# Performance work log

Hardware: AMD Instinct MI355X
Metric: run time of the kernel (lower is better)

The kernel has to match this reference:

```python
import jax, jax.numpy as jnp
import numpy as np

N_USERS = 100000
N_ITEMS = 50000
N_NODES = N_USERS + N_ITEMS
EMB_DIM = 64
N_EDGES = 4000000
N_LAYERS = 3
BATCH = 4096


def setup_inputs() -> dict:
    key = jax.random.key(0)
    k = jax.random.split(key, 7)
    return {
        "user_emb": jax.random.normal(k[0], (N_USERS, EMB_DIM), dtype=jnp.float32) * 0.1,
        "item_emb": jax.random.normal(k[1], (N_ITEMS, EMB_DIM), dtype=jnp.float32) * 0.1,
        "vals": jax.random.uniform(k[2], (N_EDGES,), dtype=jnp.float32),
        "src": jax.random.randint(k[3], (N_EDGES,), 0, N_NODES, dtype=jnp.int32),
        "dst": jax.random.randint(k[4], (N_EDGES,), 0, N_NODES, dtype=jnp.int32),
        "users": jax.random.randint(k[5], (BATCH,), 0, N_USERS, dtype=jnp.int32),
        "items": jax.random.randint(k[6], (BATCH,), 0, N_ITEMS, dtype=jnp.int32),
    }


def _propagate(user_emb, item_emb, vals, src, dst):
    # all_emb: [N, D]; sparse adjacency A given as COO (src -> dst, weight vals)
    all_emb = jnp.concatenate([user_emb, item_emb], axis=0)
    acc = all_emb  # running sum over layers (layer 0 included)
    emb = all_emb
    for _ in range(N_LAYERS):
        # SpMM: out[d] = sum_{e: dst[e]==d} vals[e] * emb[src[e]]
        msgs = vals[:, None] * emb[src]               # [E, D]
        emb = jax.ops.segment_sum(msgs, dst, num_segments=N_NODES)
        acc = acc + emb
    light_out = acc / jnp.float32(N_LAYERS + 1)       # mean over stacked layers
    return light_out[:N_USERS], light_out[N_USERS:]


def reference(user_emb, item_emb, vals, src, dst, users, items):
    all_users, all_items = _propagate(user_emb, item_emb, vals, src, dst)
    u = all_users[users]                              # [B, D]
    i = all_items[items]                              # [B, D]
    gamma = jnp.sum(u * i, axis=1)                    # [B]
    return gamma
```

## Files before the change

### kernel.cpp

```cpp
#include <hip/hip_runtime.h>
#include <hip/hip_bf16.h>

#define N_USERS 100000
#define N_ITEMS 50000
#define N_NODES 150000
#define DIM 64
#define N_EDGES 4000000
#define BATCH 4096

#define NBKT 512
#define BW 294
#define STRIDE 9216
#define PA_EDGES 4096
#define PA_ITER 16

__device__ __forceinline__ float blo(unsigned int u) { return __uint_as_float(u << 16); }
__device__ __forceinline__ float bhi(unsigned int u) { return __uint_as_float(u & 0xffff0000u); }
__device__ __forceinline__ unsigned int f2b(float f) {
    unsigned int x = __float_as_uint(f);
    return (x + 0x7fffu + ((x >> 16) & 1u)) >> 16;
}
__device__ __forceinline__ unsigned int pack2(float a, float b) {
    return f2b(a) | (f2b(b) << 16);
}

typedef float v2f __attribute__((ext_vector_type(2)));

__global__ void k_markcvt(const float* __restrict__ uemb, const float* __restrict__ iemb,
                          ushort* __restrict__ out, int* __restrict__ gcur) {
    int tid = blockIdx.x * blockDim.x + threadIdx.x;
    if (tid < NBKT) gcur[tid] = 0;
    int i = tid * 4;
    if (i >= N_NODES * DIM) return;
    const float* srcp = (i < N_USERS * DIM) ? (uemb + i) : (iemb + (i - N_USERS * DIM));
    float4 v;
    v.x = __builtin_nontemporal_load(srcp + 0);
    v.y = __builtin_nontemporal_load(srcp + 1);
    v.z = __builtin_nontemporal_load(srcp + 2);
    v.w = __builtin_nontemporal_load(srcp + 3);
    *(uint2*)(out + i) = make_uint2(pack2(v.x, v.y), pack2(v.z, v.w));
}

__global__ void __launch_bounds__(256, 4) k_partition(
        const int* __restrict__ src, const int* __restrict__ dst,
        const float* __restrict__ vals,
        int* __restrict__ gcur, int2* __restrict__ tmp) {
    __shared__ int cnt[NBKT];
    __shared__ int base_s[NBKT];
    __shared__ int off_s[NBKT];
    __shared__ int2 rec_s[PA_EDGES];
    __shared__ ushort bin_s[PA_EDGES];
    int t = threadIdx.x;
    for (int i = t; i < NBKT; i += 256) cnt[i] = 0;
    __syncthreads();
    size_t base = (size_t)blockIdx.x * PA_EDGES;
    int myb[PA_ITER];
    int mykey[PA_ITER];
    int myval[PA_ITER];
#pragma unroll
    for (int it = 0; it < PA_ITER; it++) {
        size_t i = base + (size_t)it * 256 + t;
        myb[it] = -1;
        if (i < N_EDGES) {
            int d = __builtin_nontemporal_load(dst + i);
            int s = __builtin_nontemporal_load(src + i);
            float v = __builtin_nontemporal_load(vals + i);
            int b = d / BW;
            int local = d - b * BW;
            myb[it] = b;
            mykey[it] = (s << 9) | local;
            myval[it] = __float_as_int(v);
            atomicAdd(&cnt[b], 1);
        }
    }
    __syncthreads();
    for (int i = t; i < NBKT; i += 256) {
        int c = cnt[i];
        base_s[i] = (c > 0) ? atomicAdd(&gcur[i], c) : 0;
    }
    if (t < 64) {
        int lane = t;
        int carry = 0;
        for (int c = 0; c < NBKT / 64; c++) {
            int i = c * 64 + lane;
            int x = cnt[i];
            int incl = x;
            for (int o = 1; o < 64; o <<= 1) {
                int y = __shfl_up(incl, o);
                if (lane >= o) incl += y;
            }
            off_s[i] = carry + incl - x;
            carry += __shfl(incl, 63);
        }
    }
    __syncthreads();
    for (int i = t; i < NBKT; i += 256) cnt[i] = 0;
    __syncthreads();
#pragma unroll
    for (int it = 0; it < PA_ITER; it++) {
        int b = myb[it];
        if (b >= 0) {
            int pos = off_s[b] + atomicAdd(&cnt[b], 1);
            rec_s[pos] = make_int2(mykey[it], myval[it]);
            bin_s[pos] = (ushort)b;
        }
    }
    __syncthreads();
    int nrec = off_s[NBKT - 1] + cnt[NBKT - 1];
    for (int i = t; i < nrec; i += 256) {
        int2 r = rec_s[i];
        int b = bin_s[i];
        tmp[(size_t)b * STRIDE + base_s[b] + (i - off_s[b])] = r;
    }
}

__global__ void k_scan(const int* __restrict__ gcur, int* __restrict__ bucket_ptr) {
    int lane = threadIdx.x;
    int carry = 0;
    for (int c = 0; c < NBKT / 64; c++) {
        int i = c * 64 + lane;
        int x = gcur[i];
        int incl = x;
        for (int off = 1; off < 64; off <<= 1) {
            int y = __shfl_up(incl, off);
            if (lane >= off) incl += y;
        }
        bucket_ptr[i] = carry + incl - x;
        carry += __shfl(incl, 63);
    }
    if (lane == 0) bucket_ptr[NBKT] = N_EDGES;
}

__global__ void k_bsort(const int2* __restrict__ tmp, const int* __restrict__ gcur,
                        const int* __restrict__ bucket_ptr, int* __restrict__ row_ptr,
                        int2* __restrict__ fin) {
    __shared__ int cnt[BW + 64];
    __shared__ int off[BW + 64];
    int b = blockIdx.x, t = threadIdx.x;
    int node0 = b * BW;
    int nodes = min(BW, N_NODES - node0);
    int gbase = bucket_ptr[b];
    int count = gcur[b];
    const int2* tb = tmp + (size_t)b * STRIDE;
    for (int i = t; i < BW + 64; i += 512) cnt[i] = 0;
    __syncthreads();
    for (int e = t; e < count; e += 512) atomicAdd(&cnt[tb[e].x & 511], 1);
    __syncthreads();
    if (t < 64) {
        int lane = t;
        int carry = 0;
        for (int c = 0; c < 5; c++) {
            int i = c * 64 + lane;
            int x = (i < nodes) ? cnt[i] : 0;
            int incl = x;
            for (int o = 1; o < 64; o <<= 1) {
                int y = __shfl_up(incl, o);
                if (lane >= o) incl += y;
            }
            if (i <= nodes) off[i] = carry + incl - x;
            carry += __shfl(incl, 63);
        }
    }
    __syncthreads();
    for (int i = t; i <= nodes; i += 512)
        if (node0 + i <= N_NODES) row_ptr[node0 + i] = gbase + off[i];
    __syncthreads();
    for (int e = t; e < count; e += 512) {
        int2 r = tb[e];
        int local = r.x & 511;
        int pos = gbase + atomicAdd(&off[local], 1);
        fin[pos] = make_int2(r.x >> 9, r.y);
    }
}


#define EDGE_FMA(r, u)                                                        \
    {                                                                         \
        float vf = __int_as_float((r).y);                                     \
        v2f vv = {vf, vf};                                                    \
        v2f f0 = {blo((u).x), bhi((u).x)};                                    \
        v2f f1 = {blo((u).y), bhi((u).y)};                                    \
        v2f f2 = {blo((u).z), bhi((u).z)};                                    \
        v2f f3 = {blo((u).w), bhi((u).w)};                                    \
        acc0 = __builtin_elementwise_fma(vv, f0, acc0);                       \
        acc1 = __builtin_elementwise_fma(vv, f1, acc1);                       \
        acc2 = __builtin_elementwise_fma(vv, f2, acc2);                       \
        acc3 = __builtin_elementwise_fma(vv, f3, acc3);                       \
    }

#define GATHER16(basec, r) (*(const uint4*)((basec) + ((((unsigned int)(r).x) << 7) | qoff)))
#define REC8(basec, i) (*(const int2*)((basec) + (((unsigned int)(i)) << 3)))

#define BURST32(basec)                                                        \
    {                                                                         \
        int e1 = e + 8, e2 = e + 16, e3 = e + 24;                             \
        int2 ra = REC8(basec, e);                                             \
        int2 rb = REC8(basec, min(e1, last));                                 \
        int2 rc = REC8(basec, min(e2, last));                                 \
        int2 rd = REC8(basec, min(e3, last));                                 \
        rb.y = (e1 < end) ? rb.y : 0;                                         \
        rc.y = (e2 < end) ? rc.y : 0;                                         \
        rd.y = (e3 < end) ? rd.y : 0;                                         \
        uint4 ua = GATHER16(einc, ra);                                        \
        uint4 ub = GATHER16(einc, rb);                                        \
        uint4 uc = GATHER16(einc, rc);                                        \
        uint4 ud = GATHER16(einc, rd);                                        \
        EDGE_FMA(ra, ua);                                                     \
        EDGE_FMA(rb, ub);                                                     \
        EDGE_FMA(rc, uc);                                                     \
        EDGE_FMA(rd, ud);                                                     \
        e += 32;                                                              \
    }

__global__ void k_spmm16(const ushort* __restrict__ ein, ushort* __restrict__ eout,
                         const int* __restrict__ row_ptr, const int2* __restrict__ fin) {
    int wave = (blockIdx.x * blockDim.x + threadIdx.x) >> 6;
    if (wave >= N_NODES) return;
    int lane = threadIdx.x & 63;
    int g = lane >> 3;
    int q = lane & 7;
    unsigned int qoff = (unsigned int)q << 4;
    const char* einc = (const char*)ein;
    const char* finc = (const char*)fin;
    int start = row_ptr[wave], end = row_ptr[wave + 1];
    int last = max(start, end - 1);
    v2f acc0 = {0.f, 0.f}, acc1 = {0.f, 0.f}, acc2 = {0.f, 0.f}, acc3 = {0.f, 0.f};
    int e = start + g;
    while (e < end) BURST32(finc);
#pragma unroll
    for (int off = 8; off < 64; off <<= 1) {
        acc0.x += __shfl_xor(acc0.x, off);
        acc0.y += __shfl_xor(acc0.y, off);
        acc1.x += __shfl_xor(acc1.x, off);
        acc1.y += __shfl_xor(acc1.y, off);
        acc2.x += __shfl_xor(acc2.x, off);
        acc2.y += __shfl_xor(acc2.y, off);
        acc3.x += __shfl_xor(acc3.x, off);
        acc3.y += __shfl_xor(acc3.y, off);
    }
    if (lane < 8) {
        uint4 p;
        p.x = pack2(acc0.x, acc0.y);
        p.y = pack2(acc1.x, acc1.y);
        p.z = pack2(acc2.x, acc2.y);
        p.w = pack2(acc3.x, acc3.y);
        *(uint4*)(eout + (size_t)wave * DIM + q * 8) = p;
    }
}

__global__ void k_samp(const ushort* __restrict__ ein, const int* __restrict__ row_ptr,
                       const int2* __restrict__ fin, const int* __restrict__ users,
                       const int* __restrict__ items, float* __restrict__ l3) {
    int slot = (blockIdx.x * blockDim.x + threadIdx.x) >> 6;
    if (slot >= 2 * BATCH) return;
    int lane = threadIdx.x & 63;
    int g = lane >> 3;
    int q = lane & 7;
    unsigned int qoff = (unsigned int)q << 4;
    const char* einc = (const char*)ein;
    const char* finc = (const char*)fin;
    int node = (slot < BATCH) ? users[slot] : (items[slot - BATCH] + N_USERS);
    int start = row_ptr[node], end = row_ptr[node + 1];
    int last = max(start, end - 1);
    v2f acc0 = {0.f, 0.f}, acc1 = {0.f, 0.f}, acc2 = {0.f, 0.f}, acc3 = {0.f, 0.f};
    int e = start + g;
    while (e < end) BURST32(finc);
#pragma unroll
    for (int off = 8; off < 64; off <<= 1) {
        acc0.x += __shfl_xor(acc0.x, off);
        acc0.y += __shfl_xor(acc0.y, off);
        acc1.x += __shfl_xor(acc1.x, off);
        acc1.y += __shfl_xor(acc1.y, off);
        acc2.x += __shfl_xor(acc2.x, off);
        acc2.y += __shfl_xor(acc2.y, off);
        acc3.x += __shfl_xor(acc3.x, off);
        acc3.y += __shfl_xor(acc3.y, off);
    }
    if (lane < 8) {
        float* row = l3 + (size_t)slot * DIM + q * 8;
        *(float4*)row = make_float4(acc0.x, acc0.y, acc1.x, acc1.y);
        *(float4*)(row + 4) = make_float4(acc2.x, acc2.y, acc3.x, acc3.y);
    }
}

__global__ void k_gacc0(const float* __restrict__ uemb, const float* __restrict__ iemb,
                        const ushort* __restrict__ emb, const int* __restrict__ users,
                        const int* __restrict__ items, float* __restrict__ accU,
                        float* __restrict__ accI) {
    int i = blockIdx.x * blockDim.x + threadIdx.x;
    if (i >= 2 * BATCH * DIM) return;
    int j = (i < BATCH * DIM) ? i : i - BATCH * DIM;
    int b = j >> 6, l = j & 63;
    if (i < BATCH * DIM) {
        int n = users[b];
        unsigned int u = emb[(size_t)n * DIM + l];
        accU[j] = uemb[(size_t)n * DIM + l] + __uint_as_float(u << 16);
    } else {
        int n = items[b];
        unsigned int u = emb[(size_t)(n + N_USERS) * DIM + l];
        accI[j] = iemb[(size_t)n * DIM + l] + __uint_as_float(u << 16);
    }
}

__global__ void k_gacc(const ushort* __restrict__ emb, const int* __restrict__ users,
                       const int* __restrict__ items, float* __restrict__ accU,
                       float* __restrict__ accI) {
    int i = blockIdx.x * blockDim.x + threadIdx.x;
    if (i >= 2 * BATCH * DIM) return;
    int j = (i < BATCH * DIM) ? i : i - BATCH * DIM;
    int b = j >> 6, l = j & 63;
    if (i < BATCH * DIM) {
        unsigned int u = emb[(size_t)users[b] * DIM + l];
        accU[j] += __uint_as_float(u << 16);
    } else {
        unsigned int u = emb[(size_t)(items[b] + N_USERS) * DIM + l];
        accI[j] += __uint_as_float(u << 16);
    }
}

__global__ void k_dot(const float* __restrict__ accU, const float* __restrict__ accI,
                      const float* __restrict__ l3, float* __restrict__ out) {
    int b = (blockIdx.x * blockDim.x + threadIdx.x) >> 6;
    if (b >= BATCH) return;
    int lane = threadIdx.x & 63;
    float aU = accU[b * 64 + lane] + l3[(size_t)b * 64 + lane];
    float aI = accI[b * 64 + lane] + l3[(size_t)(BATCH + b) * 64 + lane];
    float p = aU * aI;
    for (int off = 32; off; off >>= 1) p += __shfl_xor(p, off);
    if (lane == 0) out[b] = p * (1.0f / 16.0f);
}


extern "C" void kernel_launch(void* const* d_in, const int* in_sizes, int n_in,
                              void* d_out, int out_size, void* d_ws, size_t ws_size,
                              hipStream_t stream) {
    const float* user_emb = (const float*)d_in[0];
    const float* item_emb = (const float*)d_in[1];
    const float* vals = (const float*)d_in[2];
    const int* src = (const int*)d_in[3];
    const int* dst = (const int*)d_in[4];
    const int* users = (const int*)d_in[5];
    const int* items = (const int*)d_in[6];
    float* out = (float*)d_out;

    char* ws = (char*)d_ws;
    size_t off = 0;
    auto alloc = [&](size_t bytes) {
        char* p = ws + off;
        off += (bytes + 255) & ~(size_t)255;
        return p;
    };
    ushort* ebf0 = (ushort*)alloc((size_t)N_NODES * DIM * 2);
    ushort* ebf1 = (ushort*)alloc((size_t)N_NODES * DIM * 2);
    ushort* ebf2 = (ushort*)alloc((size_t)N_NODES * DIM * 2);
    int2* fin = (int2*)alloc((size_t)N_EDGES * 8);
    int* row_ptr = (int*)alloc((size_t)(N_NODES + 1) * 4);
    int* bucket_ptr = (int*)alloc((size_t)(NBKT + 1) * 4);
    int* gcur = (int*)alloc((size_t)NBKT * 4);
    float* l3 = (float*)alloc((size_t)2 * BATCH * DIM * 4);
    float* accU = (float*)alloc((size_t)BATCH * DIM * 4);
    float* accI = (float*)alloc((size_t)BATCH * DIM * 4);
    int2* tmp = (int2*)ebf1;

    k_markcvt<<<(N_NODES * DIM / 4 + 255) / 256, 256, 0, stream>>>(
        user_emb, item_emb, ebf0, gcur);

    int pa_blocks = (N_EDGES + PA_EDGES - 1) / PA_EDGES;
    k_partition<<<pa_blocks, 256, 0, stream>>>(src, dst, vals, gcur, tmp);
    k_scan<<<1, 64, 0, stream>>>(gcur, bucket_ptr);
    k_bsort<<<NBKT, 512, 0, stream>>>(tmp, gcur, bucket_ptr, row_ptr, fin);

    int gb = (2 * BATCH * DIM + 255) / 256;
    int spmm_blocks = (N_NODES * 64 + 255) / 256;
    k_spmm16<<<spmm_blocks, 256, 0, stream>>>(ebf0, ebf1, row_ptr, fin);
    k_gacc0<<<gb, 256, 0, stream>>>(user_emb, item_emb, ebf1, users, items, accU, accI);
    k_spmm16<<<spmm_blocks, 256, 0, stream>>>(ebf1, ebf2, row_ptr, fin);
    k_gacc<<<gb, 256, 0, stream>>>(ebf2, users, items, accU, accI);
    k_samp<<<(2 * BATCH * 64 + 255) / 256, 256, 0, stream>>>(ebf2, row_ptr, fin, users, items, l3);

    k_dot<<<(BATCH * 64 + 255) / 256, 256, 0, stream>>>(accU, accI, l3, out);
}
```

Before: 342.5 us.

## Fuse convert into partition, inline bucket scan, two rows per wave in SpMM

Merges the fp32-to-bf16 conversion into the partition kernel as extra blocks and replaces the counter-zeroing with a memset. Each bsort block now computes its own bucket base by summing the preceding counts, which removes the scan kernel. The SpMM now processes two destination rows per wave with interleaved gathers, exposing more memory-level parallelism. The cost is more registers per thread and wasted lanes when the two rows differ in length.

```diff
diff --git a/kernel.cpp b/kernel.cpp
--- a/kernel.cpp
+++ b/kernel.cpp
@@ -13,6 +13,8 @@
 #define STRIDE 9216
 #define PA_EDGES 4096
 #define PA_ITER 16
+#define PA_BLOCKS ((N_EDGES + PA_EDGES - 1) / PA_EDGES)
+#define CVT_BLOCKS (N_NODES * DIM / 4 / 256)
 
 __device__ __forceinline__ float blo(unsigned int u) { return __uint_as_float(u << 16); }
 __device__ __forceinline__ float bhi(unsigned int u) { return __uint_as_float(u & 0xffff0000u); }
@@ -26,22 +28,9 @@
 
 typedef float v2f __attribute__((ext_vector_type(2)));
 
-__global__ void k_markcvt(const float* __restrict__ uemb, const float* __restrict__ iemb,
-                          ushort* __restrict__ out, int* __restrict__ gcur) {
-    int tid = blockIdx.x * blockDim.x + threadIdx.x;
-    if (tid < NBKT) gcur[tid] = 0;
-    int i = tid * 4;
-    if (i >= N_NODES * DIM) return;
-    const float* srcp = (i < N_USERS * DIM) ? (uemb + i) : (iemb + (i - N_USERS * DIM));
-    float4 v;
-    v.x = __builtin_nontemporal_load(srcp + 0);
-    v.y = __builtin_nontemporal_load(srcp + 1);
-    v.z = __builtin_nontemporal_load(srcp + 2);
-    v.w = __builtin_nontemporal_load(srcp + 3);
-    *(uint2*)(out + i) = make_uint2(pack2(v.x, v.y), pack2(v.z, v.w));
-}
-
-__global__ void __launch_bounds__(256, 4) k_partition(
+__global__ void __launch_bounds__(256, 4) k_cvtpart(
+        const float* __restrict__ uemb, const float* __restrict__ iemb,
+        ushort* __restrict__ ebf0,
         const int* __restrict__ src, const int* __restrict__ dst,
         const float* __restrict__ vals,
         int* __restrict__ gcur, int2* __restrict__ tmp) {
@@ -51,6 +40,19 @@
     __shared__ int2 rec_s[PA_EDGES];
     __shared__ ushort bin_s[PA_EDGES];
     int t = threadIdx.x;
+    if (blockIdx.x >= PA_BLOCKS) {
+        int tid = (blockIdx.x - PA_BLOCKS) * 256 + t;
+        int i = tid * 4;
+        if (i >= N_NODES * DIM) return;
+        const float* srcp = (i < N_USERS * DIM) ? (uemb + i) : (iemb + (i - N_USERS * DIM));
+        float4 v;
+        v.x = __builtin_nontemporal_load(srcp + 0);
+        v.y = __builtin_nontemporal_load(srcp + 1);
+        v.z = __builtin_nontemporal_load(srcp + 2);
+        v.w = __builtin_nontemporal_load(srcp + 3);
+        *(uint2*)(ebf0 + i) = make_uint2(pack2(v.x, v.y), pack2(v.z, v.w));
+        return;
+    }
     for (int i = t; i < NBKT; i += 256) cnt[i] = 0;
     __syncthreads();
     size_t base = (size_t)blockIdx.x * PA_EDGES;
@@ -114,36 +116,29 @@
     }
 }
 
-__global__ void k_scan(const int* __restrict__ gcur, int* __restrict__ bucket_ptr) {
-    int lane = threadIdx.x;
-    int carry = 0;
-    for (int c = 0; c < NBKT / 64; c++) {
-        int i = c * 64 + lane;
-        int x = gcur[i];
-        int incl = x;
-        for (int off = 1; off < 64; off <<= 1) {
-            int y = __shfl_up(incl, off);
-            if (lane >= off) incl += y;
-        }
-        bucket_ptr[i] = carry + incl - x;
-        carry += __shfl(incl, 63);
-    }
-    if (lane == 0) bucket_ptr[NBKT] = N_EDGES;
-}
-
 __global__ void k_bsort(const int2* __restrict__ tmp, const int* __restrict__ gcur,
-                        const int* __restrict__ bucket_ptr, int* __restrict__ row_ptr,
-                        int2* __restrict__ fin) {
+                        int* __restrict__ row_ptr, int2* __restrict__ fin) {
     __shared__ int cnt[BW + 64];
     __shared__ int off[BW + 64];
+    __shared__ int gbase_s;
     int b = blockIdx.x, t = threadIdx.x;
     int node0 = b * BW;
     int nodes = min(BW, N_NODES - node0);
-    int gbase = bucket_ptr[b];
     int count = gcur[b];
     const int2* tb = tmp + (size_t)b * STRIDE;
+    if (t < 64) {
+        int ssum = 0;
+#pragma unroll
+        for (int j = 0; j < 8; j++) {
+            int idx = t * 8 + j;
+            if (idx < b) ssum += gcur[idx];
+        }
+        for (int o = 32; o; o >>= 1) ssum += __shfl_xor(ssum, o);
+        if (t == 0) gbase_s = ssum;
+    }
     for (int i = t; i < BW + 64; i += 512) cnt[i] = 0;
     __syncthreads();
+    int gbase = gbase_s;
     for (int e = t; e < count; e += 512) atomicAdd(&cnt[tb[e].x & 511], 1);
     __syncthreads();
     if (t < 64) {
@@ -174,7 +169,7 @@
 }
 
 
-#define EDGE_FMA(r, u)                                                        \
+#define EDGE_FMA(r, u, A0, A1, A2, A3)                                        \
     {                                                                         \
         float vf = __int_as_float((r).y);                                     \
         v2f vv = {vf, vf};                                                    \
@@ -182,69 +177,98 @@
         v2f f1 = {blo((u).y), bhi((u).y)};                                    \
         v2f f2 = {blo((u).z), bhi((u).z)};                                    \
         v2f f3 = {blo((u).w), bhi((u).w)};                                    \
-        acc0 = __builtin_elementwise_fma(vv, f0, acc0);                       \
-        acc1 = __builtin_elementwise_fma(vv, f1, acc1);                       \
-        acc2 = __builtin_elementwise_fma(vv, f2, acc2);                       \
-        acc3 = __builtin_elementwise_fma(vv, f3, acc3);                       \
+        A0 = __builtin_elementwise_fma(vv, f0, A0);                           \
+        A1 = __builtin_elementwise_fma(vv, f1, A1);                           \
+        A2 = __builtin_elementwise_fma(vv, f2, A2);                           \
+        A3 = __builtin_elementwise_fma(vv, f3, A3);                           \
     }
 
 #define GATHER16(basec, r) (*(const uint4*)((basec) + ((((unsigned int)(r).x) << 7) | qoff)))
 #define REC8(basec, i) (*(const int2*)((basec) + (((unsigned int)(i)) << 3)))
 
-#define BURST32(basec)                                                        \
-    {                                                                         \
-        int e1 = e + 8, e2 = e + 16, e3 = e + 24;                             \
-        int2 ra = REC8(basec, e);                                             \
-        int2 rb = REC8(basec, min(e1, last));                                 \
-        int2 rc = REC8(basec, min(e2, last));                                 \
-        int2 rd = REC8(basec, min(e3, last));                                 \
-        rb.y = (e1 < end) ? rb.y : 0;                                         \
-        rc.y = (e2 < end) ? rc.y : 0;                                         \
-        rd.y = (e3 < end) ? rd.y : 0;                                         \
-        uint4 ua = GATHER16(einc, ra);                                        \
-        uint4 ub = GATHER16(einc, rb);                                        \
-        uint4 uc = GATHER16(einc, rc);                                        \
-        uint4 ud = GATHER16(einc, rd);                                        \
-        EDGE_FMA(ra, ua);                                                     \
-        EDGE_FMA(rb, ub);                                                     \
-        EDGE_FMA(rc, uc);                                                     \
-        EDGE_FMA(rd, ud);                                                     \
-        e += 32;                                                              \
-    }
-
-__global__ void k_spmm16(const ushort* __restrict__ ein, ushort* __restrict__ eout,
-                         const int* __restrict__ row_ptr, const int2* __restrict__ fin) {
+__global__ void __launch_bounds__(256) k_spmm16(
+        const ushort* __restrict__ ein, ushort* __restrict__ eout,
+        const int* __restrict__ row_ptr, const int2* __restrict__ fin) {
     int wave = (blockIdx.x * blockDim.x + threadIdx.x) >> 6;
-    if (wave >= N_NODES) return;
+    if (wave >= N_NODES / 2) return;
     int lane = threadIdx.x & 63;
     int g = lane >> 3;
     int q = lane & 7;
     unsigned int qoff = (unsigned int)q << 4;
     const char* einc = (const char*)ein;
     const char* finc = (const char*)fin;
-    int start = row_ptr[wave], end = row_ptr[wave + 1];
-    int last = max(start, end - 1);
-    v2f acc0 = {0.f, 0.f}, acc1 = {0.f, 0.f}, acc2 = {0.f, 0.f}, acc3 = {0.f, 0.f};
-    int e = start + g;
-    while (e < end) BURST32(finc);
+    int n0 = wave * 2;
+    int s0 = row_ptr[n0];
+    int m0 = row_ptr[n0 + 1];
+    int m1 = row_ptr[n0 + 2];
+    int last0 = max(s0, m0 - 1);
+    int last1 = max(m0, m1 - 1);
+    v2f A0 = {0.f, 0.f}, A1 = {0.f, 0.f}, A2 = {0.f, 0.f}, A3 = {0.f, 0.f};
+    v2f B0 = {0.f, 0.f}, B1 = {0.f, 0.f}, B2 = {0.f, 0.f}, B3 = {0.f, 0.f};
+    int ea = s0 + g, eb = m0 + g;
+    while (ea < m0 || eb < m1) {
+        int2 ra0 = REC8(finc, min(ea, last0));
+        int2 ra1 = REC8(finc, min(ea + 8, last0));
+        int2 ra2 = REC8(finc, min(ea + 16, last0));
+        int2 ra3 = REC8(finc, min(ea + 24, last0));
+        int2 rb0 = REC8(finc, min(eb, last1));
+        int2 rb1 = REC8(finc, min(eb + 8, last1));
+        int2 rb2 = REC8(finc, min(eb + 16, last1));
+        int2 rb3 = REC8(finc, min(eb + 24, last1));
+        ra0.y = (ea < m0) ? ra0.y : 0;
+        ra1.y = (ea + 8 < m0) ? ra1.y : 0;
+        ra2.y = (ea + 16 < m0) ? ra2.y : 0;
+        ra3.y = (ea + 24 < m0) ? ra3.y : 0;
+        rb0.y = (eb < m1) ? rb0.y : 0;
+        rb1.y = (eb + 8 < m1) ? rb1.y : 0;
+        rb2.y = (eb + 16 < m1) ? rb2.y : 0;
+        rb3.y = (eb + 24 < m1) ? rb3.y : 0;
+        uint4 ua0 = GATHER16(einc, ra0);
+        uint4 ua1 = GATHER16(einc, ra1);
+        uint4 ua2 = GATHER16(einc, ra2);
+        uint4 ua3 = GATHER16(einc, ra3);
+        uint4 ub0 = GATHER16(einc, rb0);
+        uint4 ub1 = GATHER16(einc, rb1);
+        uint4 ub2 = GATHER16(einc, rb2);
+        uint4 ub3 = GATHER16(einc, rb3);
+        EDGE_FMA(ra0, ua0, A0, A1, A2, A3);
+        EDGE_FMA(ra1, ua1, A0, A1, A2, A3);
+        EDGE_FMA(ra2, ua2, A0, A1, A2, A3);
+        EDGE_FMA(ra3, ua3, A0, A1, A2, A3);
+        EDGE_FMA(rb0, ub0, B0, B1, B2, B3);
+        EDGE_FMA(rb1, ub1, B0, B1, B2, B3);
+        EDGE_FMA(rb2, ub2, B0, B1, B2, B3);
+        EDGE_FMA(rb3, ub3, B0, B1, B2, B3);
+        ea += 32;
+        eb += 32;
+    }
 #pragma unroll
     for (int off = 8; off < 64; off <<= 1) {
-        acc0.x += __shfl_xor(acc0.x, off);
-        acc0.y += __shfl_xor(acc0.y, off);
-        acc1.x += __shfl_xor(acc1.x, off);
-        acc1.y += __shfl_xor(acc1.y, off);
-        acc2.x += __shfl_xor(acc2.x, off);
-        acc2.y += __shfl_xor(acc2.y, off);
-        acc3.x += __shfl_xor(acc3.x, off);
-        acc3.y += __shfl_xor(acc3.y, off);
-    }
-    if (lane < 8) {
+        A0.x += __shfl_xor(A0.x, off);
+        A0.y += __shfl_xor(A0.y, off);
+        A1.x += __shfl_xor(A1.x, off);
+        A1.y += __shfl_xor(A1.y, off);
+        A2.x += __shfl_xor(A2.x, off);
+        A2.y += __shfl_xor(A2.y, off);
+        A3.x += __shfl_xor(A3.x, off);
+        A3.y += __shfl_xor(A3.y, off);
+        B0.x += __shfl_xor(B0.x, off);
+        B0.y += __shfl_xor(B0.y, off);
+        B1.x += __shfl_xor(B1.x, off);
+        B1.y += __shfl_xor(B1.y, off);
+        B2.x += __shfl_xor(B2.x, off);
+        B2.y += __shfl_xor(B2.y, off);
+        B3.x += __shfl_xor(B3.x, off);
+        B3.y += __shfl_xor(B3.y, off);
+    }
+    if (lane < 16) {
+        bool r0 = lane < 8;
         uint4 p;
-        p.x = pack2(acc0.x, acc0.y);
-        p.y = pack2(acc1.x, acc1.y);
-        p.z = pack2(acc2.x, acc2.y);
-        p.w = pack2(acc3.x, acc3.y);
-        *(uint4*)(eout + (size_t)wave * DIM + q * 8) = p;
+        p.x = r0 ? pack2(A0.x, A0.y) : pack2(B0.x, B0.y);
+        p.y = r0 ? pack2(A1.x, A1.y) : pack2(B1.x, B1.y);
+        p.z = r0 ? pack2(A2.x, A2.y) : pack2(B2.x, B2.y);
+        p.w = r0 ? pack2(A3.x, A3.y) : pack2(B3.x, B3.y);
+        *(uint4*)(eout + (size_t)n0 * DIM + (size_t)(lane & 15) * 8) = p;
     }
 }
 
@@ -262,24 +286,42 @@
     int node = (slot < BATCH) ? users[slot] : (items[slot - BATCH] + N_USERS);
     int start = row_ptr[node], end = row_ptr[node + 1];
     int last = max(start, end - 1);
-    v2f acc0 = {0.f, 0.f}, acc1 = {0.f, 0.f}, acc2 = {0.f, 0.f}, acc3 = {0.f, 0.f};
+    v2f A0 = {0.f, 0.f}, A1 = {0.f, 0.f}, A2 = {0.f, 0.f}, A3 = {0.f, 0.f};
     int e = start + g;
-    while (e < end) BURST32(finc);
+    while (e < end) {
+        int e1 = e + 8, e2 = e + 16, e3 = e + 24;
+        int2 ra = REC8(finc, e);
+        int2 rb = REC8(finc, min(e1, last));
+        int2 rc = REC8(finc, min(e2, last));
+        int2 rd = REC8(finc, min(e3, last));
+        rb.y = (e1 < end) ? rb.y : 0;
+        rc.y = (e2 < end) ? rc.y : 0;
+        rd.y = (e3 < end) ? rd.y : 0;
+        uint4 ua = GATHER16(einc, ra);
+        uint4 ub = GATHER16(einc, rb);
+        uint4 uc = GATHER16(einc, rc);
+        uint4 ud = GATHER16(einc, rd);
+        EDGE_FMA(ra, ua, A0, A1, A2, A3);
+        EDGE_FMA(rb, ub, A0, A1, A2, A3);
+        EDGE_FMA(rc, uc, A0, A1, A2, A3);
+        EDGE_FMA(rd, ud, A0, A1, A2, A3);
+        e += 32;
+    }
 #pragma unroll
     for (int off = 8; off < 64; off <<= 1) {
-        acc0.x += __shfl_xor(acc0.x, off);
-        acc0.y += __shfl_xor(acc0.y, off);
-        acc1.x += __shfl_xor(acc1.x, off);
-        acc1.y += __shfl_xor(acc1.y, off);
-        acc2.x += __shfl_xor(acc2.x, off);
-        acc2.y += __shfl_xor(acc2.y, off);
-        acc3.x += __shfl_xor(acc3.x, off);
-        acc3.y += __shfl_xor(acc3.y, off);
+        A0.x += __shfl_xor(A0.x, off);
+        A0.y += __shfl_xor(A0.y, off);
+        A1.x += __shfl_xor(A1.x, off);
+        A1.y += __shfl_xor(A1.y, off);
+        A2.x += __shfl_xor(A2.x, off);
+        A2.y += __shfl_xor(A2.y, off);
+        A3.x += __shfl_xor(A3.x, off);
+        A3.y += __shfl_xor(A3.y, off);
     }
     if (lane < 8) {
         float* row = l3 + (size_t)slot * DIM + q * 8;
-        *(float4*)row = make_float4(acc0.x, acc0.y, acc1.x, acc1.y);
-        *(float4*)(row + 4) = make_float4(acc2.x, acc2.y, acc3.x, acc3.y);
+        *(float4*)row = make_float4(A0.x, A0.y, A1.x, A1.y);
+        *(float4*)(row + 4) = make_float4(A2.x, A2.y, A3.x, A3.y);
     }
 }
 
@@ -355,23 +397,20 @@
     ushort* ebf2 = (ushort*)alloc((size_t)N_NODES * DIM * 2);
     int2* fin = (int2*)alloc((size_t)N_EDGES * 8);
     int* row_ptr = (int*)alloc((size_t)(N_NODES + 1) * 4);
-    int* bucket_ptr = (int*)alloc((size_t)(NBKT + 1) * 4);
     int* gcur = (int*)alloc((size_t)NBKT * 4);
     float* l3 = (float*)alloc((size_t)2 * BATCH * DIM * 4);
     float* accU = (float*)alloc((size_t)BATCH * DIM * 4);
     float* accI = (float*)alloc((size_t)BATCH * DIM * 4);
     int2* tmp = (int2*)ebf1;
 
-    k_markcvt<<<(N_NODES * DIM / 4 + 255) / 256, 256, 0, stream>>>(
-        user_emb, item_emb, ebf0, gcur);
-
-    int pa_blocks = (N_EDGES + PA_EDGES - 1) / PA_EDGES;
-    k_partition<<<pa_blocks, 256, 0, stream>>>(src, dst, vals, gcur, tmp);
-    k_scan<<<1, 64, 0, stream>>>(gcur, bucket_ptr);
-    k_bsort<<<NBKT, 512, 0, stream>>>(tmp, gcur, bucket_ptr, row_ptr, fin);
+    hipMemsetAsync(gcur, 0, (size_t)NBKT * 4, stream);
+
+    k_cvtpart<<<PA_BLOCKS + CVT_BLOCKS, 256, 0, stream>>>(
+        user_emb, item_emb, ebf0, src, dst, vals, gcur, tmp);
+    k_bsort<<<NBKT, 512, 0, stream>>>(tmp, gcur, row_ptr, fin);
 
     int gb = (2 * BATCH * DIM + 255) / 256;
-    int spmm_blocks = (N_NODES * 64 + 255) / 256;
+    int spmm_blocks = (N_NODES / 2 * 64 + 255) / 256;
     k_spmm16<<<spmm_blocks, 256, 0, stream>>>(ebf0, ebf1, row_ptr, fin);
     k_gacc0<<<gb, 256, 0, stream>>>(user_emb, item_emb, ebf1, users, items, accU, accI);
     k_spmm16<<<spmm_blocks, 256, 0, stream>>>(ebf1, ebf2, row_ptr, fin);
```

Measured after the change: 338.9 us. No clear change (-1.1%).
